# Optimization experiments

Measured on AMD Instinct MI355X. Metric: run time of the kernel, lower is better.

The kernel has to match this reference:

```python
import jax, jax.numpy as jnp
import numpy as np

N_NODES = 100000
HIDDEN = 128
N_EDGES = 1000000


def setup_inputs() -> dict:
    key = jax.random.key(0)
    k1, k2, k3, k4 = jax.random.split(key, 4)
    z = jax.random.normal(k1, (N_NODES, HIDDEN), dtype=jnp.float32)
    edge_label_index = jax.random.randint(k2, (2, N_EDGES), 0, N_NODES, dtype=jnp.int64)
    # Kaiming-ish scaled init for the two Linear layers (lin1: 2H->H, lin2: H->1)
    W1 = jax.random.normal(k3, (2 * HIDDEN, HIDDEN), dtype=jnp.float32) / np.sqrt(2 * HIDDEN)
    b1 = jnp.zeros((HIDDEN,), dtype=jnp.float32)
    W2 = jax.random.normal(k4, (HIDDEN, 1), dtype=jnp.float32) / np.sqrt(HIDDEN)
    b2 = jnp.zeros((1,), dtype=jnp.float32)
    return {"z": z, "edge_label_index": edge_label_index, "W1": W1, "b1": b1, "W2": W2, "b2": b2}


def reference(z, edge_label_index, W1, b1, W2, b2):
    row, col = edge_label_index[0], edge_label_index[1]
    # gather endpoint embeddings and concat: [E, 2H]
    h = jnp.concatenate([z[row], z[col]], axis=-1)
    h = jax.nn.relu(h @ W1 + b1)          # [E, H]
    out = h @ W2 + b2                     # [E, 1]
    return out.reshape(-1)
```

## Files before the change

### kernel.cpp

```cpp
#include <hip/hip_runtime.h>
#include <hip/hip_bf16.h>
#include <stdint.h>

#define HIDDEN 128
#define LDS_STRIDE 136

typedef __attribute__((ext_vector_type(8))) short short8;
typedef __attribute__((ext_vector_type(4))) unsigned uint4v;
typedef __attribute__((ext_vector_type(4))) float float4v;
typedef __attribute__((ext_vector_type(2))) float float2v;
typedef __attribute__((ext_vector_type(2))) unsigned uint2v;

static __device__ __forceinline__ unsigned short f2bf(float f) {
    union { float f; unsigned u; } v; v.f = f;
    unsigned r = (v.u + 0x7FFFu + ((v.u >> 16) & 1u)) >> 16;
    return (unsigned short)r;
}

static __device__ __forceinline__ unsigned pack2bf(float f0, float f1) {
    unsigned u0 = __float_as_uint(f0) + 0x8000u;
    unsigned u1 = __float_as_uint(f1) + 0x8000u;
    return __builtin_amdgcn_perm(u1, u0, 0x07060302u);
}

static __device__ __forceinline__ short8 pack8(float4v lo, float4v hi) {
    uint4v u;
    u[0] = pack2bf(lo[0], lo[1]);
    u[1] = pack2bf(lo[2], lo[3]);
    u[2] = pack2bf(hi[0], hi[1]);
    u[3] = pack2bf(hi[2], hi[3]);
    return *(short8*)&u;
}

__global__ void prep_wt(const float* __restrict__ W1, const float* __restrict__ b1,
                        const float* __restrict__ W2,
                        unsigned short* __restrict__ Wt,
                        float* __restrict__ b1p, float* __restrict__ W2p,
                        const int* __restrict__ eli, int E, unsigned M,
                        int* __restrict__ cnt) {
    __shared__ int hh[64];
    int t = threadIdx.x;
    if (t < 64) hh[t] = 0;

    int idx = blockIdx.x * blockDim.x + t;
    if (idx < 256 * 128) {
        int j = idx >> 7, k = idx & 127;
        float v = (j < 128) ? W1[k * 128 + j] : W1[(128 + k) * 128 + (j - 128)];
        Wt[idx] = f2bf(v);
    }
    if (idx < 128) {
        int m = idx >> 3, tt = idx & 7;
        int jj = tt * 16 + m;
        b1p[idx] = b1[jj];
        W2p[idx] = W2[jj];
    }
    __syncthreads();
    for (int i = idx; i < E; i += gridDim.x * blockDim.x) {
        int r = eli[i], c = eli[E + i];
        int b = (int)(__umulhi((unsigned)r, M) * 8 + __umulhi((unsigned)c, M));
        atomicAdd(&hh[b], 1);
    }
    __syncthreads();
    if (t < 64 && hh[t] > 0) atomicAdd(&cnt[t], hh[t]);
}

__global__ void bucket_scan(const int* __restrict__ cnt, int* __restrict__ boff,
                            int* __restrict__ cur) {
    if (threadIdx.x == 0) {
        int acc = 0;
        for (int i = 0; i < 64; ++i) { boff[i] = acc; cur[i] = acc; acc += cnt[i]; }
        boff[64] = acc;
    }
}

__global__ void edge_scatter(const int* __restrict__ eli, int E, unsigned M,
                             int* __restrict__ cur, int* __restrict__ sr,
                             unsigned long long* __restrict__ sce) {
    __shared__ int hh[64];
    __shared__ int base[64];
    const int CH = 2048;
    int t = threadIdx.x;
    int start = blockIdx.x * CH;
    if (start >= E) return;
    int end = min(start + CH, E);

    if (t < 64) hh[t] = 0;
    __syncthreads();
    for (int i = start + t; i < end; i += 256) {
        int r = eli[i], c = eli[E + i];
        int b = (int)(__umulhi((unsigned)r, M) * 8 + __umulhi((unsigned)c, M));
        atomicAdd(&hh[b], 1);
    }
    __syncthreads();
    if (t < 64) {
        base[t] = (hh[t] > 0) ? atomicAdd(&cur[t], hh[t]) : 0;
        hh[t] = 0;
    }
    __syncthreads();
    for (int i = start + t; i < end; i += 256) {
        int r = eli[i], c = eli[E + i];
        int b = (int)(__umulhi((unsigned)r, M) * 8 + __umulhi((unsigned)c, M));
        int p = base[b] + atomicAdd(&hh[b], 1);
        sr[p]  = r;
        sce[p] = ((unsigned long long)(unsigned)i << 32) | (unsigned)c;
    }
}

__global__ __launch_bounds__(512) void node_gemm(
        const float* __restrict__ z, const unsigned short* __restrict__ Wt,
        const float* __restrict__ b1p,
        unsigned char* __restrict__ Qi, float* __restrict__ sA, float* __restrict__ sB,
        int n_nodes) {
    __shared__ unsigned short Wl[128 * LDS_STRIDE];

    int tid  = threadIdx.x;
    int h    = blockIdx.x & 1;

    #pragma unroll
    for (int i = 0; i < 4; ++i) {
        int chunk = tid + i * 512;
        int c  = chunk >> 4;
        int k0 = (chunk & 15) * 8;
        short8 v = *(const short8*)(Wt + h * 16384 + chunk * 8);
        *(short8*)(Wl + c * LDS_STRIDE + k0) = v;
    }
    __syncthreads();

    int lane = tid & 63;
    int wave = tid >> 6;
    int m    = lane & 15;
    int quad = lane >> 4;

    float4v b1a = (float4v)(0.0f), b1b = (float4v)(0.0f);
    if (h == 0) {
        b1a = *(const float4v*)(b1p + m * 8);
        b1b = *(const float4v*)(b1p + m * 8 + 4);
    }
    float* sArr = (h == 0) ? sA : sB;

    int nTiles = (n_nodes + 15) >> 4;
    int tileStride = (gridDim.x >> 1) * 8;

    for (int tile = (blockIdx.x >> 1) * 8 + wave; tile < nTiles; tile += tileStride) {
        int nodebase = tile * 16;
        int row = nodebase + m;

        short8 a[4];
        {
            bool ok = row < n_nodes;
            const float* zp = z + (size_t)row * HIDDEN + quad * 8;
            #pragma unroll
            for (int s = 0; s < 4; ++s) {
                float4v z0 = ok ? *(const float4v*)(zp + s * 32)     : (float4v)(0.0f);
                float4v z1 = ok ? *(const float4v*)(zp + s * 32 + 4) : (float4v)(0.0f);
                a[s] = pack8(z0, z1);
            }
        }

        float4v acc[8];
        #pragma unroll
        for (int t = 0; t < 8; ++t) acc[t] = (float4v)(0.0f);

        #pragma unroll
        for (int t = 0; t < 8; ++t) {
            const unsigned short* wp = Wl + (t * 16 + m) * LDS_STRIDE + quad * 8;
            #pragma unroll
            for (int s = 0; s < 4; ++s) {
                short8 b = *(const short8*)(wp + s * 32);
                acc[t] = __builtin_amdgcn_mfma_f32_16x16x32_bf16(a[s], b, acc[t], 0, 0, 0);
            }
        }

        #pragma unroll
        for (int r = 0; r < 4; ++r) {
            int node = nodebase + quad * 4 + r;
            float v[8];
            v[0] = acc[0][r] + b1a[0]; v[1] = acc[1][r] + b1a[1];
            v[2] = acc[2][r] + b1a[2]; v[3] = acc[3][r] + b1a[3];
            v[4] = acc[4][r] + b1b[0]; v[5] = acc[5][r] + b1b[1];
            v[6] = acc[6][r] + b1b[2]; v[7] = acc[7][r] + b1b[3];

            float amax = fabsf(v[0]);
            #pragma unroll
            for (int t = 1; t < 8; ++t) amax = fmaxf(amax, fabsf(v[t]));
            amax = fmaxf(amax, __shfl_xor(amax, 1));
            amax = fmaxf(amax, __shfl_xor(amax, 2));
            amax = fmaxf(amax, __shfl_xor(amax, 4));
            amax = fmaxf(amax, __shfl_xor(amax, 8));
            amax = fmaxf(amax, 1e-30f);

            float inv = 126.5f * __builtin_amdgcn_rcpf(amax);
            float s   = amax * (1.0f / 126.5f);

            unsigned d0 = 0, d1 = 0;
            #pragma unroll
            for (int t = 0; t < 4; ++t) {
                int q = (int)rintf(fmaf(v[t], inv, 128.0f));
                d0 |= ((unsigned)q & 255u) << (8 * t);
            }
            #pragma unroll
            for (int t = 0; t < 4; ++t) {
                int q = (int)rintf(fmaf(v[4 + t], inv, 128.0f));
                d1 |= ((unsigned)q & 255u) << (8 * t);
            }

            if (node < n_nodes) {
                uint2v pk; pk[0] = d0; pk[1] = d1;
                *(uint2v*)(Qi + (size_t)node * 256 + h * 128 + m * 8) = pk;
                if (m == 0) sArr[node] = s;
            }
        }
    }
}

static __device__ __forceinline__ float edge_dot8(uint2v u1, uint2v u2,
                                                  float a1, float a2,
                                                  float4v wA, float4v wB) {
    float off = -128.0f * (a1 + a2);
    float acc = 0.0f;
    unsigned da = u1[0], db = u2[0];
    #pragma unroll
    for (int k = 0; k < 4; ++k) {
        float af = (float)((da >> (8 * k)) & 255u);
        float bf = (float)((db >> (8 * k)) & 255u);
        float v = fmaf(a2, bf, fmaf(a1, af, off));
        v = fmaxf(v, 0.0f);
        acc = fmaf(v, wA[k], acc);
    }
    da = u1[1]; db = u2[1];
    #pragma unroll
    for (int k = 0; k < 4; ++k) {
        float af = (float)((da >> (8 * k)) & 255u);
        float bf = (float)((db >> (8 * k)) & 255u);
        float v = fmaf(a2, bf, fmaf(a1, af, off));
        v = fmaxf(v, 0.0f);
        acc = fmaf(v, wB[k], acc);
    }
    return acc;
}

__global__ __launch_bounds__(256) void edge_kernel_b(
        const int* __restrict__ sr, const unsigned long long* __restrict__ sce,
        const int* __restrict__ boff,
        const unsigned char* __restrict__ Qi,
        const float* __restrict__ sA, const float* __restrict__ sB,
        const float* __restrict__ W2p, const float* __restrict__ b2,
        float* __restrict__ out) {
    int g      = threadIdx.x >> 4;
    int lane16 = threadIdx.x & 15;
    int j0 = lane16 * 8;

    float4v wA = *(const float4v*)(W2p + j0);
    float4v wB = *(const float4v*)(W2p + j0 + 4);
    float bias2 = b2[0];

    int x  = blockIdx.x & 7;
    int kb = blockIdx.x >> 3;
    int K  = gridDim.x >> 3;
    int rs = boff[x * 8];
    int re = boff[x * 8 + 8];

    for (int base = rs + kb * 64; base < re; base += K * 64) {
        int idx_r[4], idx_c[4], oe[4];
        bool okf[4];
        #pragma unroll
        for (int i = 0; i < 4; ++i) {
            int e = base + i * 16 + g;
            bool ok = e < re;
            okf[i] = ok;
            int ee = ok ? e : base;
            idx_r[i] = sr[ee];
            unsigned long long ce = sce[ee];
            idx_c[i] = (int)(unsigned)(ce & 0xFFFFFFFFull);
            oe[i]    = (int)(unsigned)(ce >> 32);
        }

        uint2v u1[4], u2[4];
        float s1[4], s2[4];
        #pragma unroll
        for (int i = 0; i < 4; ++i) {
            u1[i] = *(const uint2v*)(Qi + (size_t)idx_r[i] * 256 + j0);
            u2[i] = *(const uint2v*)(Qi + (size_t)idx_c[i] * 256 + 128 + j0);
            s1[i] = sA[idx_r[i]];
            s2[i] = sB[idx_c[i]];
        }

        #pragma unroll
        for (int i = 0; i < 4; ++i) {
            float acc = edge_dot8(u1[i], u2[i], s1[i], s2[i], wA, wB);
            acc += __shfl_xor(acc, 1);
            acc += __shfl_xor(acc, 2);
            acc += __shfl_xor(acc, 4);
            acc += __shfl_xor(acc, 8);
            if (lane16 == 0 && okf[i]) out[oe[i]] = acc + bias2;
        }
    }
}

__global__ __launch_bounds__(256) void edge_kernel(
        const int* __restrict__ eli, const unsigned char* __restrict__ Qi,
        const float* __restrict__ sA, const float* __restrict__ sB,
        const float* __restrict__ W2p, const float* __restrict__ b2,
        float* __restrict__ out, int E) {
    int g      = threadIdx.x >> 4;
    int lane16 = threadIdx.x & 15;
    int j0 = lane16 * 8;

    float4v wA = *(const float4v*)(W2p + j0);
    float4v wB = *(const float4v*)(W2p + j0 + 4);
    float bias2 = b2[0];

    int e0 = blockIdx.x * 64 + g;

    int idx_r[4], idx_c[4];
    #pragma unroll
    for (int i = 0; i < 4; ++i) {
        int e = e0 + i * 16;
        idx_r[i] = (e < E) ? eli[e]     : 0;
        idx_c[i] = (e < E) ? eli[E + e] : 0;
    }

    uint2v u1[4], u2[4];
    float s1[4], s2[4];
    #pragma unroll
    for (int i = 0; i < 4; ++i) {
        u1[i] = *(const uint2v*)(Qi + (size_t)idx_r[i] * 256 + j0);
        u2[i] = *(const uint2v*)(Qi + (size_t)idx_c[i] * 256 + 128 + j0);
        s1[i] = sA[idx_r[i]];
        s2[i] = sB[idx_c[i]];
    }

    #pragma unroll
    for (int i = 0; i < 4; ++i) {
        float acc = edge_dot8(u1[i], u2[i], s1[i], s2[i], wA, wB);
        acc += __shfl_xor(acc, 1);
        acc += __shfl_xor(acc, 2);
        acc += __shfl_xor(acc, 4);
        acc += __shfl_xor(acc, 8);
        int e = e0 + i * 16;
        if (lane16 == 0 && e < E) out[e] = acc + bias2;
    }
}

extern "C" void kernel_launch(void* const* d_in, const int* in_sizes, int n_in,
                              void* d_out, int out_size, void* d_ws, size_t ws_size,
                              hipStream_t stream) {
    const float* z   = (const float*)d_in[0];
    const int*   eli = (const int*)d_in[1];
    const float* W1  = (const float*)d_in[2];
    const float* b1  = (const float*)d_in[3];
    const float* W2  = (const float*)d_in[4];
    const float* b2  = (const float*)d_in[5];
    int n_nodes = in_sizes[0] / HIDDEN;
    int E       = in_sizes[1] / 2;
    float* out  = (float*)d_out;

    unsigned M = (unsigned)((((unsigned long long)8 << 32) + n_nodes - 1) / (unsigned)n_nodes);

    size_t off = 0;
    unsigned char* Qi  = (unsigned char*)d_ws;                 off += (size_t)n_nodes * 256;
    unsigned short* Wt = (unsigned short*)((char*)d_ws + off); off += 256 * 128 * 2;
    float* b1p = (float*)((char*)d_ws + off);                  off += 128 * 4;
    float* W2p = (float*)((char*)d_ws + off);                  off += 128 * 4;
    float* sA  = (float*)((char*)d_ws + off);                  off += (size_t)n_nodes * 4;
    float* sB  = (float*)((char*)d_ws + off);                  off += (size_t)n_nodes * 4;
    off = (off + 255) & ~(size_t)255;
    int* sr  = (int*)((char*)d_ws + off);                      off += (size_t)E * 4;
    off = (off + 7) & ~(size_t)7;
    unsigned long long* sce = (unsigned long long*)((char*)d_ws + off); off += (size_t)E * 8;
    int* cnt  = (int*)((char*)d_ws + off);                     off += 64 * 4;
    int* boff = (int*)((char*)d_ws + off);                     off += 65 * 4;
    int* cur  = (int*)((char*)d_ws + off);                     off += 64 * 4;
    bool use_sort = (off <= ws_size);

    if (use_sort) {
        hipMemsetAsync(cnt, 0, 64 * 4, stream);
        prep_wt<<<128, 256, 0, stream>>>(W1, b1, W2, Wt, b1p, W2p, eli, E, M, cnt);
        bucket_scan<<<1, 64, 0, stream>>>(cnt, boff, cur);
        edge_scatter<<<(E + 2047) / 2048, 256, 0, stream>>>(eli, E, M, cur, sr, sce);
        node_gemm<<<1024, 512, 0, stream>>>(z, Wt, b1p, Qi, sA, sB, n_nodes);
        edge_kernel_b<<<2048, 256, 0, stream>>>(sr, sce, boff, Qi, sA, sB, W2p, b2, out);
    } else {
        prep_wt<<<128, 256, 0, stream>>>(W1, b1, W2, Wt, b1p, W2p, eli, 0, M, (int*)Qi);
        node_gemm<<<1024, 512, 0, stream>>>(z, Wt, b1p, Qi, sA, sB, n_nodes);
        edge_kernel<<<(E + 63) / 64, 256, 0, stream>>>(eli, Qi, sA, sB, W2p, b2, out, E);
    }
}
```

Before: 191.6 us.

## Double-buffer edge gathers, pack dot math, parallel bucket scan, larger scatter chunks

The bucketed edge kernel now prefetches the next batch of indices and quantized embeddings into registers while the current batch is computed, to hide gather latency. The per-edge dot product is rewritten with float2 vector operations, which may map to packed FP32 instructions. The single-thread bucket scan becomes a wavefront shuffle scan, and edge_scatter chunks grow from 2048 to 4096 edges, which halves its block count. The prefetch doubles register use for the gathered data, so occupancy may drop.

```diff
diff --git a/kernel.cpp b/kernel.cpp
--- a/kernel.cpp
+++ b/kernel.cpp
@@ -66,11 +66,18 @@
 
 __global__ void bucket_scan(const int* __restrict__ cnt, int* __restrict__ boff,
                             int* __restrict__ cur) {
-    if (threadIdx.x == 0) {
-        int acc = 0;
-        for (int i = 0; i < 64; ++i) { boff[i] = acc; cur[i] = acc; acc += cnt[i]; }
-        boff[64] = acc;
-    }
+    int t = threadIdx.x;
+    int v = cnt[t];
+    int s = v;
+    #pragma unroll
+    for (int d = 1; d < 64; d <<= 1) {
+        int u = __shfl_up(s, d, 64);
+        if (t >= d) s += u;
+    }
+    int excl = s - v;
+    boff[t] = excl;
+    cur[t]  = excl;
+    if (t == 63) boff[64] = s;
 }
 
 __global__ void edge_scatter(const int* __restrict__ eli, int E, unsigned M,
@@ -78,7 +85,7 @@
                              unsigned long long* __restrict__ sce) {
     __shared__ int hh[64];
     __shared__ int base[64];
-    const int CH = 2048;
+    const int CH = 4096;
     int t = threadIdx.x;
     int start = blockIdx.x * CH;
     if (start >= E) return;
@@ -215,28 +222,59 @@
 
 static __device__ __forceinline__ float edge_dot8(uint2v u1, uint2v u2,
                                                   float a1, float a2,
-                                                  float4v wA, float4v wB) {
-    float off = -128.0f * (a1 + a2);
-    float acc = 0.0f;
-    unsigned da = u1[0], db = u2[0];
-    #pragma unroll
-    for (int k = 0; k < 4; ++k) {
-        float af = (float)((da >> (8 * k)) & 255u);
-        float bf = (float)((db >> (8 * k)) & 255u);
-        float v = fmaf(a2, bf, fmaf(a1, af, off));
-        v = fmaxf(v, 0.0f);
-        acc = fmaf(v, wA[k], acc);
-    }
-    da = u1[1]; db = u2[1];
-    #pragma unroll
-    for (int k = 0; k < 4; ++k) {
-        float af = (float)((da >> (8 * k)) & 255u);
-        float bf = (float)((db >> (8 * k)) & 255u);
-        float v = fmaf(a2, bf, fmaf(a1, af, off));
-        v = fmaxf(v, 0.0f);
-        acc = fmaf(v, wB[k], acc);
-    }
-    return acc;
+                                                  const float2v* w2) {
+    float offs = -128.0f * (a1 + a2);
+    float2v off2; off2[0] = offs; off2[1] = offs;
+    float2v a1v;  a1v[0] = a1;   a1v[1] = a1;
+    float2v a2v;  a2v[0] = a2;   a2v[1] = a2;
+    float2v acc2; acc2[0] = 0.0f; acc2[1] = 0.0f;
+    #pragma unroll
+    for (int d = 0; d < 2; ++d) {
+        unsigned da = u1[d], db = u2[d];
+        #pragma unroll
+        for (int p = 0; p < 2; ++p) {
+            float2v af, bf;
+            af[0] = (float)((da >> (16 * p))     & 255u);
+            af[1] = (float)((da >> (16 * p + 8)) & 255u);
+            bf[0] = (float)((db >> (16 * p))     & 255u);
+            bf[1] = (float)((db >> (16 * p + 8)) & 255u);
+            float2v t = a2v * bf + off2;
+            float2v s = a1v * af + t;
+            s[0] = fmaxf(s[0], 0.0f);
+            s[1] = fmaxf(s[1], 0.0f);
+            acc2 = acc2 + s * w2[2 * d + p];
+        }
+    }
+    return acc2[0] + acc2[1];
+}
+
+struct Batch {
+    uint2v u1[4], u2[4];
+    float  s1[4], s2[4];
+    int    oe[4];
+    bool   ok[4];
+};
+
+static __device__ __forceinline__ void load_batch(
+        int base, int g, int j0, int re,
+        const int* __restrict__ sr, const unsigned long long* __restrict__ sce,
+        const unsigned char* __restrict__ Qi,
+        const float* __restrict__ sA, const float* __restrict__ sB, Batch& B) {
+    #pragma unroll
+    for (int i = 0; i < 4; ++i) {
+        int e = base + i * 16 + g;
+        bool ok = e < re;
+        B.ok[i] = ok;
+        int ee = ok ? e : (re - 1);
+        int r = sr[ee];
+        unsigned long long ce = sce[ee];
+        int c = (int)(unsigned)(ce & 0xFFFFFFFFull);
+        B.oe[i] = (int)(unsigned)(ce >> 32);
+        B.u1[i] = *(const uint2v*)(Qi + (size_t)r * 256 + j0);
+        B.u2[i] = *(const uint2v*)(Qi + (size_t)c * 256 + 128 + j0);
+        B.s1[i] = sA[r];
+        B.s2[i] = sB[c];
+    }
 }
 
 __global__ __launch_bounds__(256) void edge_kernel_b(
@@ -250,8 +288,9 @@
     int lane16 = threadIdx.x & 15;
     int j0 = lane16 * 8;
 
-    float4v wA = *(const float4v*)(W2p + j0);
-    float4v wB = *(const float4v*)(W2p + j0 + 4);
+    float2v w2[4];
+    #pragma unroll
+    for (int k = 0; k < 4; ++k) w2[k] = ((const float2v*)(W2p + j0))[k];
     float bias2 = b2[0];
 
     int x  = blockIdx.x & 7;
@@ -259,41 +298,30 @@
     int K  = gridDim.x >> 3;
     int rs = boff[x * 8];
     int re = boff[x * 8 + 8];
-
-    for (int base = rs + kb * 64; base < re; base += K * 64) {
-        int idx_r[4], idx_c[4], oe[4];
-        bool okf[4];
+    int stride = K * 64;
+    int base = rs + kb * 64;
+    if (base >= re) return;
+
+    Batch cur, nxt;
+    load_batch(base, g, j0, re, sr, sce, Qi, sA, sB, cur);
+
+    while (base < re) {
+        int nb = base + stride;
+        bool has = nb < re;
+        if (has) load_batch(nb, g, j0, re, sr, sce, Qi, sA, sB, nxt);
+
         #pragma unroll
         for (int i = 0; i < 4; ++i) {
-            int e = base + i * 16 + g;
-            bool ok = e < re;
-            okf[i] = ok;
-            int ee = ok ? e : base;
-            idx_r[i] = sr[ee];
-            unsigned long long ce = sce[ee];
-            idx_c[i] = (int)(unsigned)(ce & 0xFFFFFFFFull);
-            oe[i]    = (int)(unsigned)(ce >> 32);
-        }
-
-        uint2v u1[4], u2[4];
-        float s1[4], s2[4];
-        #pragma unroll
-        for (int i = 0; i < 4; ++i) {
-            u1[i] = *(const uint2v*)(Qi + (size_t)idx_r[i] * 256 + j0);
-            u2[i] = *(const uint2v*)(Qi + (size_t)idx_c[i] * 256 + 128 + j0);
-            s1[i] = sA[idx_r[i]];
-            s2[i] = sB[idx_c[i]];
-        }
-
-        #pragma unroll
-        for (int i = 0; i < 4; ++i) {
-            float acc = edge_dot8(u1[i], u2[i], s1[i], s2[i], wA, wB);
+            float acc = edge_dot8(cur.u1[i], cur.u2[i], cur.s1[i], cur.s2[i], w2);
             acc += __shfl_xor(acc, 1);
             acc += __shfl_xor(acc, 2);
             acc += __shfl_xor(acc, 4);
             acc += __shfl_xor(acc, 8);
-            if (lane16 == 0 && okf[i]) out[oe[i]] = acc + bias2;
+            if (lane16 == 0 && cur.ok[i]) out[cur.oe[i]] = acc + bias2;
         }
+
+        base = nb;
+        if (has) cur = nxt;
     }
 }
 
@@ -306,8 +334,9 @@
     int lane16 = threadIdx.x & 15;
     int j0 = lane16 * 8;
 
-    float4v wA = *(const float4v*)(W2p + j0);
-    float4v wB = *(const float4v*)(W2p + j0 + 4);
+    float2v w2[4];
+    #pragma unroll
+    for (int k = 0; k < 4; ++k) w2[k] = ((const float2v*)(W2p + j0))[k];
     float bias2 = b2[0];
 
     int e0 = blockIdx.x * 64 + g;
@@ -332,7 +361,7 @@
 
     #pragma unroll
     for (int i = 0; i < 4; ++i) {
-        float acc = edge_dot8(u1[i], u2[i], s1[i], s2[i], wA, wB);
+        float acc = edge_dot8(u1[i], u2[i], s1[i], s2[i], w2);
         acc += __shfl_xor(acc, 1);
         acc += __shfl_xor(acc, 2);
         acc += __shfl_xor(acc, 4);
@@ -377,7 +406,7 @@
         hipMemsetAsync(cnt, 0, 64 * 4, stream);
         prep_wt<<<128, 256, 0, stream>>>(W1, b1, W2, Wt, b1p, W2p, eli, E, M, cnt);
         bucket_scan<<<1, 64, 0, stream>>>(cnt, boff, cur);
-        edge_scatter<<<(E + 2047) / 2048, 256, 0, stream>>>(eli, E, M, cur, sr, sce);
+        edge_scatter<<<(E + 4095) / 4096, 256, 0, stream>>>(eli, E, M, cur, sr, sce);
         node_gemm<<<1024, 512, 0, stream>>>(z, Wt, b1p, Qi, sA, sB, n_nodes);
         edge_kernel_b<<<2048, 256, 0, stream>>>(sr, sce, boff, Qi, sA, sB, W2p, b2, out);
     } else {
```

Result: no change. 193.1 us (+0.8%).
